# Performance work log

Measured on AMD Instinct MI355X. Metric: run time of the kernel, lower is better.

The kernel has to match this reference:

```python
import jax, jax.numpy as jnp
import numpy as np

D_MODEL = 1024
N_HEAD = 16
HEAD_DIM = D_MODEL // N_HEAD


def setup_inputs() -> dict:
    key = jax.random.key(0)
    ks = jax.random.split(key, 5)
    B, T, C = 2, 2048, D_MODEL
    s = 1.0 / np.sqrt(C)
    return {
        "x": jax.random.normal(ks[0], (B, T, C), dtype=jnp.float32),
        "Wq": jax.random.normal(ks[1], (C, D_MODEL), dtype=jnp.float32) * s,
        "Wk": jax.random.normal(ks[2], (C, D_MODEL), dtype=jnp.float32) * s,
        "Wv": jax.random.normal(ks[3], (C, D_MODEL), dtype=jnp.float32) * s,
        "Wo": jax.random.normal(ks[4], (D_MODEL, D_MODEL), dtype=jnp.float32) * s,
        "bo": jnp.zeros((D_MODEL,), dtype=jnp.float32),
    }


def reference(x, Wq, Wk, Wv, Wo, bo):
    B, T, C = x.shape
    H, Dh = N_HEAD, HEAD_DIM
    # QKV projections (no bias, matching qkv_bias=False), split into heads
    q = (x @ Wq).reshape(B, T, H, Dh).transpose(0, 2, 1, 3)  # [B,H,T,Dh]
    k = (x @ Wk).reshape(B, T, H, Dh).transpose(0, 2, 1, 3)
    v = (x @ Wv).reshape(B, T, H, Dh).transpose(0, 2, 1, 3)
    # scaled causal attention scores [B,H,T,T]
    omega = jnp.einsum("bhqd,bhkd->bhqk", q, k)
    causal = jnp.tril(jnp.ones((T, T), dtype=bool))  # True where allowed
    omega = jnp.where(causal, omega, -jnp.inf)
    att = jax.nn.softmax(omega / np.sqrt(Dh), axis=-1)
    # dropout p=0.0 -> identity
    ctx = jnp.einsum("bhqk,bhkd->bhqd", att, v)  # [B,H,T,Dh]
    ctx = ctx.transpose(0, 2, 1, 3).reshape(B, T, C)
    return ctx @ Wo + bo
```

## Files before the change

kernel.cpp:

```cpp
#include <hip/hip_runtime.h>
#include <hip/hip_bf16.h>

typedef __attribute__((ext_vector_type(8))) short short8;
typedef __attribute__((ext_vector_type(4))) float f32x4;
typedef __attribute__((ext_vector_type(16))) float f32x16;
typedef __attribute__((ext_vector_type(4))) unsigned short u16x4;

#define D_MODEL 1024
#define N_HEAD 16
#define HEAD_DIM 64
#define T_SEQ 2048
#define BATCH 2
#define M_TOK (BATCH * T_SEQ)
#define QKV_STRIDE ((size_t)M_TOK * D_MODEL)

__device__ __forceinline__ unsigned short f2bf(float f) {
    union { float f; unsigned u; } v; v.f = f;
    unsigned r = (v.u + 0x7fffu + ((v.u >> 16) & 1u)) >> 16;
    return (unsigned short)r;
}

__device__ __forceinline__ float exp2_fast(float x) {
    float r;
    asm("v_exp_f32 %0, %1" : "=v"(r) : "v"(x));
    return r;
}

__device__ __forceinline__ void load16_lds(const unsigned short* g, unsigned short* l) {
    __builtin_amdgcn_global_load_lds(
        (const __attribute__((address_space(1))) unsigned int*)(g),
        (__attribute__((address_space(3))) unsigned int*)(l),
        16, 0, 0);
}

__global__ __launch_bounds__(256) void cast_x(const float* __restrict__ in,
                                              unsigned short* __restrict__ out, int n4) {
    int i = blockIdx.x * 256 + threadIdx.x;
    if (i < n4) {
        float4 v = ((const float4*)in)[i];
        u16x4 o;
        o.x = f2bf(v.x); o.y = f2bf(v.y); o.z = f2bf(v.z); o.w = f2bf(v.w);
        ((u16x4*)out)[i] = o;
    }
}

__global__ __launch_bounds__(256) void transpose_cast4(
    const float* __restrict__ w0, const float* __restrict__ w1,
    const float* __restrict__ w2, const float* __restrict__ w3,
    unsigned short* __restrict__ o0, unsigned short* __restrict__ o1,
    unsigned short* __restrict__ o2, unsigned short* __restrict__ o3)
{
    __shared__ float tile[32][33];
    const float* in; unsigned short* outT;
    switch (blockIdx.z) {
        case 0: in = w0; outT = o0; break;
        case 1: in = w1; outT = o1; break;
        case 2: in = w2; outT = o2; break;
        default: in = w3; outT = o3; break;
    }
    const int R = 1024, C = 1024;
    const int r0 = blockIdx.x * 32, c0 = blockIdx.y * 32;
    const int tx = threadIdx.x & 31, ty = threadIdx.x >> 5;
    #pragma unroll
    for (int jj = 0; jj < 32; jj += 8)
        tile[ty + jj][tx] = in[(size_t)(r0 + ty + jj) * C + c0 + tx];
    __syncthreads();
    #pragma unroll
    for (int jj = 0; jj < 32; jj += 8)
        outT[(size_t)(c0 + ty + jj) * R + r0 + tx] = f2bf(tile[tx][ty + jj]);
}

#define BM 128
#define BN 128
#define BK 32
__global__ __launch_bounds__(256) void gemm_bf16(
    const unsigned short* __restrict__ A,
    const unsigned short* __restrict__ Bt,
    void* __restrict__ outp,
    const float* __restrict__ bias,
    int M, int N, int K, int mode)
{
    __shared__ unsigned short lds_a[2][BM * BK];
    __shared__ unsigned short lds_b[2][BN * BK];
    const int tid = threadIdx.x;
    const int w = tid >> 6, l = tid & 63, lo = l & 15, hi = l >> 4;
    const int wm = w >> 1, wn = w & 1;
    const size_t arow0 = (size_t)blockIdx.x * BM;
    const size_t brow0 = (size_t)blockIdx.y * BN;

    f32x4 acc[4][4];
    #pragma unroll
    for (int i = 0; i < 4; ++i)
        #pragma unroll
        for (int j = 0; j < 4; ++j)
            acc[i][j] = (f32x4){0.f, 0.f, 0.f, 0.f};

    const int ch0 = tid, ch1 = 256 + tid;
    const int r0c = ch0 >> 2, c0c = (ch0 & 3) * 8;
    const int r1c = ch1 >> 2, c1c = (ch1 & 3) * 8;
    const unsigned short* Ab0 = A + (arow0 + r0c) * K + c0c;
    const unsigned short* Ab1 = A + (arow0 + r1c) * K + c1c;
    const unsigned short* Bb0 = Bt + (brow0 + r0c) * K + c0c;
    const unsigned short* Bb1 = Bt + (brow0 + r1c) * K + c1c;
    const int woff0 = (0 * 256 + w * 64) * 8, woff1 = (1 * 256 + w * 64) * 8;

#define GSTAGE(BUF, KOFF)                                  \
    do {                                                   \
        load16_lds(Ab0 + (KOFF), lds_a[BUF] + woff0);      \
        load16_lds(Ab1 + (KOFF), lds_a[BUF] + woff1);      \
        load16_lds(Bb0 + (KOFF), lds_b[BUF] + woff0);      \
        load16_lds(Bb1 + (KOFF), lds_b[BUF] + woff1);      \
    } while (0)

    GSTAGE(0, 0);
    int cur = 0;
    for (int k0 = 0; k0 < K; k0 += BK) {
        __syncthreads();
        if (k0 + BK < K) GSTAGE(cur ^ 1, k0 + BK);
        short8 af[4], bfr[4];
        #pragma unroll
        for (int i = 0; i < 4; ++i)
            af[i] = *(const short8*)(lds_a[cur] + (wm * 64 + i * 16 + lo) * BK + 8 * hi);
        #pragma unroll
        for (int j = 0; j < 4; ++j)
            bfr[j] = *(const short8*)(lds_b[cur] + (wn * 64 + j * 16 + lo) * BK + 8 * hi);
        #pragma unroll
        for (int i = 0; i < 4; ++i)
            #pragma unroll
            for (int j = 0; j < 4; ++j)
                acc[i][j] = __builtin_amdgcn_mfma_f32_16x16x32_bf16(af[i], bfr[j], acc[i][j], 0, 0, 0);
        cur ^= 1;
    }
#undef GSTAGE

    const int m00 = (int)arow0 + wm * 64;
    const int n00 = (int)brow0 + wn * 64;
    if (mode == 1) {
        unsigned short* out = (unsigned short*)outp;
        #pragma unroll
        for (int i = 0; i < 4; ++i)
            #pragma unroll
            for (int j = 0; j < 4; ++j) {
                const int nbase = n00 + j * 16;
                const int qkv = nbase >> 10;
                #pragma unroll
                for (int e = 0; e < 4; ++e) {
                    const int m = m00 + i * 16 + 4 * hi + e;
                    const int n = nbase + lo;
                    const int b = m >> 11, t = m & 2047;
                    const int h = (n >> 6) & 15, d = n & 63;
                    const int bh = (b << 4) + h;
                    float v = acc[i][j][e];
                    size_t off;
                    if (qkv == 0) {
                        off = ((size_t)bh * T_SEQ + t) * HEAD_DIM + d;
                    } else if (qkv == 1) {
                        v *= 0.18033688f;
                        off = QKV_STRIDE + ((size_t)bh * T_SEQ + t) * HEAD_DIM + d;
                    } else {
                        off = 2 * QKV_STRIDE + ((size_t)bh * HEAD_DIM + d) * T_SEQ + t;
                    }
                    out[off] = f2bf(v);
                }
            }
    } else {
        float* out = (float*)outp;
        #pragma unroll
        for (int i = 0; i < 4; ++i)
            #pragma unroll
            for (int j = 0; j < 4; ++j)
                #pragma unroll
                for (int e = 0; e < 4; ++e) {
                    const int m = m00 + i * 16 + 4 * hi + e;
                    const int n = n00 + j * 16 + lo;
                    out[(size_t)m * N + n] = acc[i][j][e] + bias[n];
                }
    }
}

__global__ __launch_bounds__(256) void attn_fwd(
    const unsigned short* __restrict__ QKV,
    unsigned short* __restrict__ ctx)
{
    const int qi = (int)(gridDim.x - 1 - blockIdx.x);
    const int bh = blockIdx.y;
    const int b = bh >> 4, h = bh & 15;
    const int tid = threadIdx.x;
    const int wid = tid >> 6;
    const int l = tid & 63;
    const int l31 = l & 31, hi1 = l >> 5;
    const int q0w = qi * 128 + wid * 32;
    const int q = q0w + l31;

    const unsigned short* Qb = QKV + (size_t)bh * T_SEQ * HEAD_DIM;
    const unsigned short* Kb = QKV + QKV_STRIDE + (size_t)bh * T_SEQ * HEAD_DIM;
    const unsigned short* Vb = QKV + 2 * QKV_STRIDE + (size_t)bh * HEAD_DIM * T_SEQ;

    __shared__ unsigned short kbuf[2][128 * 64];
    __shared__ unsigned short vbuf[2][64 * 128];

    short8 qf[4];
    #pragma unroll
    for (int st = 0; st < 4; ++st)
        qf[st] = *(const short8*)(Qb + (size_t)q * 64 + 16 * st + 8 * hi1);

    f32x16 o0, o1;
    #pragma unroll
    for (int r = 0; r < 16; ++r) { o0[r] = 0.f; o1[r] = 0.f; }
    float mrun = -3e38f, lsum = 0.f;

#define STAGE(B, SI)                                                                     \
    do {                                                                                 \
        _Pragma("unroll")                                                                \
        for (int it = 0; it < 4; ++it) {                                                 \
            const int D = it * 256 + tid;                                                \
            const int kr = D >> 3, kc = D & 7;                                           \
            load16_lds(Kb + (size_t)((SI) * 128 + kr) * 64 + ((kc ^ (kr & 7)) * 8),      \
                       &kbuf[B][(it * 256 + wid * 64) * 8]);                             \
            const int vr = D >> 4, vc = D & 15;                                          \
            load16_lds(Vb + (size_t)vr * T_SEQ + (SI) * 128 + ((vc ^ (vr & 7)) * 8),     \
                       &vbuf[B][(it * 256 + wid * 64) * 8]);                             \
        }                                                                                \
    } while (0)

    STAGE(0, 0);
    int cur = 0;
    for (int si = 0; si <= qi; ++si) {
        __syncthreads();
        if (si < qi) STAGE(cur ^ 1, si + 1);
        #pragma unroll
        for (int kbl = 0; kbl < 4; ++kbl) {
            const int kbase = si * 128 + kbl * 32;
            if (kbase <= q0w) {
                short8 kf[4];
                #pragma unroll
                for (int st = 0; st < 4; ++st) {
                    const int r = kbl * 32 + l31;
                    const int cc = (2 * st + hi1) ^ (r & 7);
                    kf[st] = *(const short8*)&kbuf[cur][r * 64 + cc * 8];
                }
                f32x16 s_;
                #pragma unroll
                for (int r = 0; r < 16; ++r) s_[r] = 0.f;
                s_ = __builtin_amdgcn_mfma_f32_32x32x16_bf16(kf[0], qf[0], s_, 0, 0, 0);
                s_ = __builtin_amdgcn_mfma_f32_32x32x16_bf16(kf[1], qf[1], s_, 0, 0, 0);
                s_ = __builtin_amdgcn_mfma_f32_32x32x16_bf16(kf[2], qf[2], s_, 0, 0, 0);
                s_ = __builtin_amdgcn_mfma_f32_32x32x16_bf16(kf[3], qf[3], s_, 0, 0, 0);
                if (kbase == q0w) {
                    #pragma unroll
                    for (int r = 0; r < 16; ++r)
                        if ((r & 3) + 8 * (r >> 2) + 4 * hi1 > l31) s_[r] = -3e38f;
                }
                float pm = s_[0];
                #pragma unroll
                for (int r = 1; r < 16; ++r) pm = fmaxf(pm, s_[r]);
                pm = fmaxf(pm, __shfl_xor(pm, 32));
                if (__any(pm > mrun + 8.0f)) {
                    const float mnew = fmaxf(mrun, pm);
                    const float sc = exp2_fast(mrun - mnew);
                    mrun = mnew;
                    lsum *= sc;
                    #pragma unroll
                    for (int r = 0; r < 16; ++r) { o0[r] *= sc; o1[r] *= sc; }
                }
                float p[16];
                #pragma unroll
                for (int r = 0; r < 16; ++r) p[r] = exp2_fast(s_[r] - mrun);
                float rs = (((p[0] + p[1]) + (p[2] + p[3])) + ((p[4] + p[5]) + (p[6] + p[7])))
                         + (((p[8] + p[9]) + (p[10] + p[11])) + ((p[12] + p[13]) + (p[14] + p[15])));
                rs += __shfl_xor(rs, 32);
                lsum += rs;
                unsigned c0, c1, c2, c3, c4, c5, c6, c7;
                asm volatile("v_cvt_pk_bf16_f32 %0, %1, %2" : "=v"(c0) : "v"(p[0]),  "v"(p[1]));
                asm volatile("v_cvt_pk_bf16_f32 %0, %1, %2" : "=v"(c1) : "v"(p[2]),  "v"(p[3]));
                asm volatile("v_cvt_pk_bf16_f32 %0, %1, %2" : "=v"(c2) : "v"(p[4]),  "v"(p[5]));
                asm volatile("v_cvt_pk_bf16_f32 %0, %1, %2" : "=v"(c3) : "v"(p[6]),  "v"(p[7]));
                asm volatile("v_cvt_pk_bf16_f32 %0, %1, %2" : "=v"(c4) : "v"(p[8]),  "v"(p[9]));
                asm volatile("v_cvt_pk_bf16_f32 %0, %1, %2" : "=v"(c5) : "v"(p[10]), "v"(p[11]));
                asm volatile("v_cvt_pk_bf16_f32 %0, %1, %2" : "=v"(c6) : "v"(p[12]), "v"(p[13]));
                asm volatile("v_cvt_pk_bf16_f32 %0, %1, %2" : "=v"(c7) : "v"(p[14]), "v"(p[15]));
                asm volatile("v_permlane32_swap_b32 %0, %1" : "+v"(c0), "+v"(c2));
                asm volatile("v_permlane32_swap_b32 %0, %1" : "+v"(c1), "+v"(c3));
                asm volatile("v_permlane32_swap_b32 %0, %1" : "+v"(c4), "+v"(c6));
                asm volatile("v_permlane32_swap_b32 %0, %1" : "+v"(c5), "+v"(c7));
                union { short8 v; unsigned u[4]; } pb0, pb1;
                pb0.u[0] = c0; pb0.u[1] = c1; pb0.u[2] = c2; pb0.u[3] = c3;
                pb1.u[0] = c4; pb1.u[1] = c5; pb1.u[2] = c6; pb1.u[3] = c7;
                const int d0 = l31, d1 = 32 + l31;
                const int cv00 = (kbl * 4 + 0 + hi1) ^ (d0 & 7);
                const int cv01 = (kbl * 4 + 2 + hi1) ^ (d0 & 7);
                const int cv10 = (kbl * 4 + 0 + hi1) ^ (d1 & 7);
                const int cv11 = (kbl * 4 + 2 + hi1) ^ (d1 & 7);
                const short8 v00 = *(const short8*)&vbuf[cur][d0 * 128 + cv00 * 8];
                const short8 v01 = *(const short8*)&vbuf[cur][d0 * 128 + cv01 * 8];
                const short8 v10 = *(const short8*)&vbuf[cur][d1 * 128 + cv10 * 8];
                const short8 v11 = *(const short8*)&vbuf[cur][d1 * 128 + cv11 * 8];
                o0 = __builtin_amdgcn_mfma_f32_32x32x16_bf16(v00, pb0.v, o0, 0, 0, 0);
                o0 = __builtin_amdgcn_mfma_f32_32x32x16_bf16(v01, pb1.v, o0, 0, 0, 0);
                o1 = __builtin_amdgcn_mfma_f32_32x32x16_bf16(v10, pb0.v, o1, 0, 0, 0);
                o1 = __builtin_amdgcn_mfma_f32_32x32x16_bf16(v11, pb1.v, o1, 0, 0, 0);
            }
        }
        cur ^= 1;
    }
#undef STAGE

    const float inv = 1.0f / lsum;
    unsigned short* crow = ctx + (size_t)(b * T_SEQ + q) * D_MODEL + h * 64;
    #pragma unroll
    for (int rq = 0; rq < 4; ++rq) {
        const int dd = 8 * rq + 4 * hi1;
        u16x4 ov;
        ov.x = f2bf(o0[4 * rq + 0] * inv);
        ov.y = f2bf(o0[4 * rq + 1] * inv);
        ov.z = f2bf(o0[4 * rq + 2] * inv);
        ov.w = f2bf(o0[4 * rq + 3] * inv);
        *(u16x4*)(crow + dd) = ov;
        u16x4 ov1;
        ov1.x = f2bf(o1[4 * rq + 0] * inv);
        ov1.y = f2bf(o1[4 * rq + 1] * inv);
        ov1.z = f2bf(o1[4 * rq + 2] * inv);
        ov1.w = f2bf(o1[4 * rq + 3] * inv);
        *(u16x4*)(crow + 32 + dd) = ov1;
    }
}

extern "C" void kernel_launch(void* const* d_in, const int* in_sizes, int n_in,
                              void* d_out, int out_size, void* d_ws, size_t ws_size,
                              hipStream_t stream)
{
    const float* x  = (const float*)d_in[0];
    const float* Wq = (const float*)d_in[1];
    const float* Wk = (const float*)d_in[2];
    const float* Wv = (const float*)d_in[3];
    const float* Wo = (const float*)d_in[4];
    const float* bo = (const float*)d_in[5];
    float* out = (float*)d_out;

    char* ws = (char*)d_ws;
    unsigned short* x_bf = (unsigned short*)(ws);
    unsigned short* WqT  = (unsigned short*)(ws + (8u << 20));
    unsigned short* WkT  = (unsigned short*)(ws + (10u << 20));
    unsigned short* WvT  = (unsigned short*)(ws + (12u << 20));
    unsigned short* WoT  = (unsigned short*)(ws + (14u << 20));
    unsigned short* QKV  = (unsigned short*)(ws + (16u << 20));
    unsigned short* ctx  = (unsigned short*)(ws + (40u << 20));
    (void)in_sizes; (void)n_in; (void)out_size; (void)ws_size;

    cast_x<<<dim3((M_TOK * D_MODEL / 4 + 255) / 256), 256, 0, stream>>>(x, x_bf, M_TOK * D_MODEL / 4);
    transpose_cast4<<<dim3(32, 32, 4), 256, 0, stream>>>(Wq, Wk, Wv, Wo, WqT, WkT, WvT, WoT);

    gemm_bf16<<<dim3(M_TOK / BM, 3072 / BN), 256, 0, stream>>>(
        x_bf, WqT, QKV, nullptr, M_TOK, 3072, D_MODEL, 1);

    attn_fwd<<<dim3(T_SEQ / 128, BATCH * N_HEAD), 256, 0, stream>>>(QKV, ctx);

    gemm_bf16<<<dim3(M_TOK / BM, D_MODEL / BN), 256, 0, stream>>>(
        ctx, WoT, out, bo, M_TOK, D_MODEL, D_MODEL, 2);
}
```

Baseline: 211.1 us.

## Write V row-major from QKV GEMM, transpose separately; narrow output GEMM tile

The QKV GEMM epilogue now writes V in the same row-major [bh,t,d] layout as Q and K, which removes the strided transposed scatter stores. A separate LDS-tiled transpose kernel then builds the V^T layout that attention expects, in reused workspace. The output projection GEMM is templated to a 64-wide N tile, which doubles its block count for better CU occupancy at 1024 columns. The cost is an extra kernel launch plus an extra read and write pass over V.

```diff
diff --git a/kernel.cpp b/kernel.cpp
--- a/kernel.cpp
+++ b/kernel.cpp
@@ -70,9 +70,25 @@
         outT[(size_t)(c0 + ty + jj) * R + r0 + tx] = f2bf(tile[tx][ty + jj]);
 }
 
+__global__ __launch_bounds__(256) void transpose_v(const unsigned short* __restrict__ in,
+                                                   unsigned short* __restrict__ out) {
+    __shared__ unsigned short tile[32][33];
+    const int t0 = blockIdx.x * 32, d0 = blockIdx.y * 32, bh = blockIdx.z;
+    const int tx = threadIdx.x & 31, ty = threadIdx.x >> 5;
+    const unsigned short* ib = in + (size_t)bh * T_SEQ * HEAD_DIM;
+    unsigned short* ob = out + (size_t)bh * HEAD_DIM * T_SEQ;
+    #pragma unroll
+    for (int jj = 0; jj < 32; jj += 8)
+        tile[ty + jj][tx] = ib[(size_t)(t0 + ty + jj) * HEAD_DIM + d0 + tx];
+    __syncthreads();
+    #pragma unroll
+    for (int jj = 0; jj < 32; jj += 8)
+        ob[(size_t)(d0 + ty + jj) * T_SEQ + t0 + tx] = tile[tx][ty + jj];
+}
+
 #define BM 128
-#define BN 128
 #define BK 32
+template <int BNv>
 __global__ __launch_bounds__(256) void gemm_bf16(
     const unsigned short* __restrict__ A,
     const unsigned short* __restrict__ Bt,
@@ -80,19 +96,21 @@
     const float* __restrict__ bias,
     int M, int N, int K, int mode)
 {
+    constexpr int WN = BNv / 2;
+    constexpr int NJ = WN / 16;
     __shared__ unsigned short lds_a[2][BM * BK];
-    __shared__ unsigned short lds_b[2][BN * BK];
+    __shared__ unsigned short lds_b[2][BNv * BK];
     const int tid = threadIdx.x;
     const int w = tid >> 6, l = tid & 63, lo = l & 15, hi = l >> 4;
     const int wm = w >> 1, wn = w & 1;
     const size_t arow0 = (size_t)blockIdx.x * BM;
-    const size_t brow0 = (size_t)blockIdx.y * BN;
-
-    f32x4 acc[4][4];
+    const size_t brow0 = (size_t)blockIdx.y * BNv;
+
+    f32x4 acc[4][NJ];
     #pragma unroll
     for (int i = 0; i < 4; ++i)
         #pragma unroll
-        for (int j = 0; j < 4; ++j)
+        for (int j = 0; j < NJ; ++j)
             acc[i][j] = (f32x4){0.f, 0.f, 0.f, 0.f};
 
     const int ch0 = tid, ch1 = 256 + tid;
@@ -104,12 +122,13 @@
     const unsigned short* Bb1 = Bt + (brow0 + r1c) * K + c1c;
     const int woff0 = (0 * 256 + w * 64) * 8, woff1 = (1 * 256 + w * 64) * 8;
 
-#define GSTAGE(BUF, KOFF)                                  \
-    do {                                                   \
-        load16_lds(Ab0 + (KOFF), lds_a[BUF] + woff0);      \
-        load16_lds(Ab1 + (KOFF), lds_a[BUF] + woff1);      \
-        load16_lds(Bb0 + (KOFF), lds_b[BUF] + woff0);      \
-        load16_lds(Bb1 + (KOFF), lds_b[BUF] + woff1);      \
+#define GSTAGE(BUF, KOFF)                                        \
+    do {                                                         \
+        load16_lds(Ab0 + (KOFF), lds_a[BUF] + woff0);            \
+        load16_lds(Ab1 + (KOFF), lds_a[BUF] + woff1);            \
+        load16_lds(Bb0 + (KOFF), lds_b[BUF] + woff0);            \
+        if constexpr (BNv == 128)                                \
+            load16_lds(Bb1 + (KOFF), lds_b[BUF] + woff1);        \
     } while (0)
 
     GSTAGE(0, 0);
@@ -117,30 +136,30 @@
     for (int k0 = 0; k0 < K; k0 += BK) {
         __syncthreads();
         if (k0 + BK < K) GSTAGE(cur ^ 1, k0 + BK);
-        short8 af[4], bfr[4];
+        short8 af[4], bfr[NJ];
         #pragma unroll
         for (int i = 0; i < 4; ++i)
             af[i] = *(const short8*)(lds_a[cur] + (wm * 64 + i * 16 + lo) * BK + 8 * hi);
         #pragma unroll
-        for (int j = 0; j < 4; ++j)
-            bfr[j] = *(const short8*)(lds_b[cur] + (wn * 64 + j * 16 + lo) * BK + 8 * hi);
+        for (int j = 0; j < NJ; ++j)
+            bfr[j] = *(const short8*)(lds_b[cur] + (wn * WN + j * 16 + lo) * BK + 8 * hi);
         #pragma unroll
         for (int i = 0; i < 4; ++i)
             #pragma unroll
-            for (int j = 0; j < 4; ++j)
+            for (int j = 0; j < NJ; ++j)
                 acc[i][j] = __builtin_amdgcn_mfma_f32_16x16x32_bf16(af[i], bfr[j], acc[i][j], 0, 0, 0);
         cur ^= 1;
     }
 #undef GSTAGE
 
     const int m00 = (int)arow0 + wm * 64;
-    const int n00 = (int)brow0 + wn * 64;
+    const int n00 = (int)brow0 + wn * WN;
     if (mode == 1) {
         unsigned short* out = (unsigned short*)outp;
         #pragma unroll
         for (int i = 0; i < 4; ++i)
             #pragma unroll
-            for (int j = 0; j < 4; ++j) {
+            for (int j = 0; j < NJ; ++j) {
                 const int nbase = n00 + j * 16;
                 const int qkv = nbase >> 10;
                 #pragma unroll
@@ -151,15 +170,9 @@
                     const int h = (n >> 6) & 15, d = n & 63;
                     const int bh = (b << 4) + h;
                     float v = acc[i][j][e];
-                    size_t off;
-                    if (qkv == 0) {
-                        off = ((size_t)bh * T_SEQ + t) * HEAD_DIM + d;
-                    } else if (qkv == 1) {
-                        v *= 0.18033688f;
-                        off = QKV_STRIDE + ((size_t)bh * T_SEQ + t) * HEAD_DIM + d;
-                    } else {
-                        off = 2 * QKV_STRIDE + ((size_t)bh * HEAD_DIM + d) * T_SEQ + t;
-                    }
+                    if (qkv == 1) v *= 0.18033688f;
+                    const size_t off = (size_t)qkv * QKV_STRIDE
+                                     + ((size_t)bh * T_SEQ + t) * HEAD_DIM + d;
                     out[off] = f2bf(v);
                 }
             }
@@ -168,7 +181,7 @@
         #pragma unroll
         for (int i = 0; i < 4; ++i)
             #pragma unroll
-            for (int j = 0; j < 4; ++j)
+            for (int j = 0; j < NJ; ++j)
                 #pragma unroll
                 for (int e = 0; e < 4; ++e) {
                     const int m = m00 + i * 16 + 4 * hi + e;
@@ -180,6 +193,7 @@
 
 __global__ __launch_bounds__(256) void attn_fwd(
     const unsigned short* __restrict__ QKV,
+    const unsigned short* __restrict__ Vt,
     unsigned short* __restrict__ ctx)
 {
     const int qi = (int)(gridDim.x - 1 - blockIdx.x);
@@ -194,7 +208,7 @@
 
     const unsigned short* Qb = QKV + (size_t)bh * T_SEQ * HEAD_DIM;
     const unsigned short* Kb = QKV + QKV_STRIDE + (size_t)bh * T_SEQ * HEAD_DIM;
-    const unsigned short* Vb = QKV + 2 * QKV_STRIDE + (size_t)bh * HEAD_DIM * T_SEQ;
+    const unsigned short* Vb = Vt + (size_t)bh * HEAD_DIM * T_SEQ;
 
     __shared__ unsigned short kbuf[2][128 * 64];
     __shared__ unsigned short vbuf[2][64 * 128];
@@ -344,17 +358,21 @@
     unsigned short* WvT  = (unsigned short*)(ws + (12u << 20));
     unsigned short* WoT  = (unsigned short*)(ws + (14u << 20));
     unsigned short* QKV  = (unsigned short*)(ws + (16u << 20));
+    unsigned short* Vraw = (unsigned short*)(ws + (32u << 20));
+    unsigned short* Vt   = (unsigned short*)(ws);
     unsigned short* ctx  = (unsigned short*)(ws + (40u << 20));
     (void)in_sizes; (void)n_in; (void)out_size; (void)ws_size;
 
     cast_x<<<dim3((M_TOK * D_MODEL / 4 + 255) / 256), 256, 0, stream>>>(x, x_bf, M_TOK * D_MODEL / 4);
     transpose_cast4<<<dim3(32, 32, 4), 256, 0, stream>>>(Wq, Wk, Wv, Wo, WqT, WkT, WvT, WoT);
 
-    gemm_bf16<<<dim3(M_TOK / BM, 3072 / BN), 256, 0, stream>>>(
+    gemm_bf16<128><<<dim3(M_TOK / BM, 3072 / 128), 256, 0, stream>>>(
         x_bf, WqT, QKV, nullptr, M_TOK, 3072, D_MODEL, 1);
 
-    attn_fwd<<<dim3(T_SEQ / 128, BATCH * N_HEAD), 256, 0, stream>>>(QKV, ctx);
-
-    gemm_bf16<<<dim3(M_TOK / BM, D_MODEL / BN), 256, 0, stream>>>(
+    transpose_v<<<dim3(T_SEQ / 32, HEAD_DIM / 32, BATCH * N_HEAD), 256, 0, stream>>>(Vraw, Vt);
+
+    attn_fwd<<<dim3(T_SEQ / 128, BATCH * N_HEAD), 256, 0, stream>>>(QKV, Vt, ctx);
+
+    gemm_bf16<64><<<dim3(M_TOK / BM, D_MODEL / 64), 256, 0, stream>>>(
         ctx, WoT, out, bo, M_TOK, D_MODEL, D_MODEL, 2);
 }
```

After: 222.7 us. +5.5%, slower.
